# Optimization experiments

Measured on AMD Instinct MI355X. Metric: run time of the kernel, lower is better.

Reference implementation:

```python
import jax, jax.numpy as jnp
import numpy as np

B, S, D, H = 8, 2048, 256, 256


def setup_inputs() -> dict:
    key = jax.random.key(0)
    ks = jax.random.split(key, 7)
    s_ih = 1.0 / np.sqrt(D)
    s_hh = 1.0 / np.sqrt(H)
    return {
        "x": jax.random.normal(ks[0], (B, S, D), dtype=jnp.float32),
        "Wih_f": jax.random.uniform(ks[1], (4 * H, D), jnp.float32, -s_ih, s_ih),
        "bih_f": jax.random.uniform(ks[2], (4 * H,), jnp.float32, -s_ih, s_ih),
        "Whh_f": jax.random.uniform(ks[3], (4 * H, H), jnp.float32, -s_hh, s_hh),
        "Wih_b": jax.random.uniform(ks[4], (4 * H, D), jnp.float32, -s_ih, s_ih),
        "bih_b": jax.random.uniform(ks[5], (4 * H,), jnp.float32, -s_ih, s_ih),
        "Whh_b": jax.random.uniform(ks[6], (4 * H, H), jnp.float32, -s_hh, s_hh),
    }


def _lstm_dir(x, Wih, bih, Whh, reverse):
    # Precompute input projection for all timesteps in one GEMM: [B,S,4H]
    b, s, _ = x.shape
    h_dim = Whh.shape[1]
    x_proj = jnp.einsum("bsd,gd->bsg", x, Wih) + bih

    def step(carry, xt):  # xt: [B,4H]
        h, c = carry
        gates = xt + h @ Whh.T
        i, f, g, o = jnp.split(gates, 4, axis=-1)
        i = jax.nn.sigmoid(i)
        f = jax.nn.sigmoid(f)
        o = jax.nn.sigmoid(o)
        g = jnp.tanh(g)
        c = f * c + i * g
        h = o * jnp.tanh(c)
        return (h, c), h

    init = (jnp.zeros((b, h_dim), x.dtype), jnp.zeros((b, h_dim), x.dtype))
    # scan over time; reverse=True processes t=S-1..0 and stacks outputs in
    # original time order, matching the torch backward loop with insert(0, .)
    _, hs = jax.lax.scan(step, init, jnp.swapaxes(x_proj, 0, 1), reverse=reverse)
    return jnp.swapaxes(hs, 0, 1)  # [B,S,H]


def reference(x, Wih_f, bih_f, Whh_f, Wih_b, bih_b, Whh_b):
    fwd = _lstm_dir(x, Wih_f, bih_f, Whh_f, reverse=False)
    bwd = _lstm_dir(x, Wih_b, bih_b, Whh_b, reverse=True)
    return jnp.concatenate([fwd, bwd], axis=-1)  # [B,S,2H]
```

## Files before the change

kernel.cpp:

```cpp
#include <hip/hip_runtime.h>
#include <hip/hip_bf16.h>
#include <stdint.h>

#define SQ   2048
#define NB   8
#define G4   1024
#define NROW 16384

typedef float f32x4 __attribute__((ext_vector_type(4)));
typedef short bf16x8 __attribute__((ext_vector_type(8)));
typedef uint32_t u32;
typedef unsigned long long u64;

__device__ __forceinline__ f32x4 mfma16(bf16x8 a, bf16x8 b, f32x4 c) {
  return __builtin_amdgcn_mfma_f32_16x16x32_bf16(a, b, c, 0, 0, 0);
}
__device__ __forceinline__ u32 pk_bf16(float lo, float hi) {
  u32 r;
  asm("v_cvt_pk_bf16_f32 %0, %1, %2" : "=v"(r) : "v"(lo), "v"(hi));
  return r;
}
__device__ __forceinline__ float bf_lo(u32 u){ union{u32 a; float f;} x; x.a = u << 16;        return x.f; }
__device__ __forceinline__ float bf_hi(u32 u){ union{u32 a; float f;} x; x.a = u & 0xffff0000u; return x.f; }

__device__ __forceinline__ float sigm(float x)   { return 1.0f / (1.0f + __expf(-x)); }
__device__ __forceinline__ float tanh_f(float x) { return 1.0f - 2.0f / (__expf(2.0f * x) + 1.0f); }

#define PIN(x) asm volatile("" : "+v"(x))

__device__ __forceinline__ u64 ld_fast(const u64* p) {
  u64 v;
  asm volatile("global_load_dwordx2 %0, %1, off sc0\n\ts_waitcnt vmcnt(0)"
               : "=v"(v) : "v"(p) : "memory");
  return v;
}
__device__ __forceinline__ void st_fast(u64* p, u64 v) {
  asm volatile("global_store_dwordx2 %0, %1, off sc0" :: "v"(p), "v"(v) : "memory");
}

__global__ __launch_bounds__(256) void xproj_gemm(
    const float* __restrict__ x,
    const float* __restrict__ WihF, const float* __restrict__ bihF,
    const float* __restrict__ WihB, const float* __restrict__ bihB,
    uint16_t* __restrict__ xp)
{
  const int dir = blockIdx.z;
  const float* Wih = dir ? WihB : WihF;
  const float* bih = dir ? bihB : bihF;
  char* xpd = (char*)xp + (size_t)dir * ((size_t)NROW * G4 * 2);

  const int g0 = blockIdx.y * 128;
  const int m0 = blockIdx.x * 128;

  __shared__ union {
    struct { short A[128 * 72]; short B[128 * 72]; } s;
    short T[128 * 136];
  } u;
  __shared__ float biasS[128];

  const int tid  = threadIdx.x;
  const int lane = tid & 63;
  const int w    = tid >> 6;
  const int wg   = w >> 1;
  const int wm   = w & 1;
  const int l15  = lane & 15;
  const int l4   = lane >> 4;

  if (tid < 128) biasS[tid] = bih[g0 + tid];

  f32x4 acc[4][4] = {};

  const int r_st = tid >> 1;
  const int half = tid & 1;
  const int mrow_st = m0 + r_st;
  const int xb = mrow_st & 7;
  const int xt = mrow_st >> 3;
  const float* xrow = x + ((size_t)xb * SQ + xt) * 256;
  const float* wrow = Wih + (size_t)(g0 + r_st) * 256;

  for (int s = 0; s < 4; ++s) {
    const int k0 = s * 64;
    __syncthreads();
    {
      const float* srcA = wrow + k0 + half * 32;
      const float* srcB = xrow + k0 + half * 32;
      short* dstA = u.s.A + r_st * 72 + half * 32;
      short* dstB = u.s.B + r_st * 72 + half * 32;
      #pragma unroll
      for (int j = 0; j < 4; ++j) {
        f32x4 a0 = *(const f32x4*)(srcA + j * 8);
        f32x4 a1 = *(const f32x4*)(srcA + j * 8 + 4);
        uint4 pa = { pk_bf16(a0.x, a0.y), pk_bf16(a0.z, a0.w),
                     pk_bf16(a1.x, a1.y), pk_bf16(a1.z, a1.w) };
        *(uint4*)(dstA + j * 8) = pa;
        f32x4 b0 = *(const f32x4*)(srcB + j * 8);
        f32x4 b1 = *(const f32x4*)(srcB + j * 8 + 4);
        uint4 pb = { pk_bf16(b0.x, b0.y), pk_bf16(b0.z, b0.w),
                     pk_bf16(b1.x, b1.y), pk_bf16(b1.z, b1.w) };
        *(uint4*)(dstB + j * 8) = pb;
      }
    }
    __syncthreads();
    #pragma unroll
    for (int kt = 0; kt < 2; ++kt) {
      bf16x8 aF[4], bF[4];
      #pragma unroll
      for (int i = 0; i < 4; ++i) {
        const int ar = wg * 64 + i * 16 + l15;
        const int br = wm * 64 + i * 16 + l15;
        aF[i] = *(const bf16x8*)(u.s.A + ar * 72 + kt * 32 + l4 * 8);
        bF[i] = *(const bf16x8*)(u.s.B + br * 72 + kt * 32 + l4 * 8);
      }
      #pragma unroll
      for (int i = 0; i < 4; ++i)
        #pragma unroll
        for (int j = 0; j < 4; ++j)
          acc[i][j] = mfma16(aF[i], bF[j], acc[i][j]);
    }
  }

  __syncthreads();
  #pragma unroll
  for (int i = 0; i < 4; ++i) {
    const f32x4 bv = *(const f32x4*)(biasS + wg * 64 + i * 16 + l4 * 4);
    #pragma unroll
    for (int j = 0; j < 4; ++j) {
      f32x4 v = acc[i][j];
      v.x += bv.x; v.y += bv.y; v.z += bv.z; v.w += bv.w;
      const int mrow = wm * 64 + j * 16 + l15;
      const int gcol = wg * 64 + i * 16 + l4 * 4;
      uint2 p; p.x = pk_bf16(v.x, v.y); p.y = pk_bf16(v.z, v.w);
      *(uint2*)(u.T + mrow * 136 + gcol) = p;
    }
  }
  __syncthreads();
  {
    const char* trow = (const char*)(u.T + r_st * 136);
    char* orow = xpd + (size_t)(m0 + r_st) * 2048 + g0 * 2;
    #pragma unroll
    for (int j = 0; j < 8; ++j) {
      const int local = half * 128 + j * 16;
      uint4 v = *(const uint4*)(trow + local);
      *(uint4*)(orow + local) = v;
    }
  }
}

template<int HALF>
__device__ __forceinline__ void lstm_body(
    const float* __restrict__ Whh, const uint16_t* __restrict__ xpd,
    float* __restrict__ out,
    u64* exf_me, u64* exs_me, const u64* exf_pt, const u64* exs_pt, int dir,
    uint16_t (*hT)[8][136], uint16_t (*hP)[8][136])
{
  const int tid  = threadIdx.x;
  const int lane = tid & 63;
  const int w    = tid >> 6;
  const int l15  = lane & 15;
  const int l4   = lane >> 4;
  const int bcl  = lane & 7;
  const int qsel = (lane >> 3) & 1;

  bf16x8 W[4][8];
  #pragma unroll
  for (int g = 0; g < 4; ++g) {
    const int row = g * 256 + HALF * 128 + w * 16 + l15;
    const float* src = Whh + (size_t)row * 256 + l4 * 8;
    #pragma unroll
    for (int kt = 0; kt < 8; ++kt) {
      f32x4 v0 = *(const f32x4*)(src + kt * 32);
      f32x4 v1 = *(const f32x4*)(src + kt * 32 + 4);
      union { bf16x8 v; u32 u[4]; } pk;
      pk.u[0] = pk_bf16(v0.x, v0.y); pk.u[1] = pk_bf16(v0.z, v0.w);
      pk.u[2] = pk_bf16(v1.x, v1.y); pk.u[3] = pk_bf16(v1.z, v1.w);
      W[g][kt] = pk.v;
      PIN(W[g][kt]);
    }
  }

  const int d0   = w * 16 + l4 * 4 + qsel * 2;
  const int word = bcl * 64 + (d0 >> 1);
  float c0 = 0.0f, c1 = 0.0f;

  u32 xq[4], xqn[4];
  {
    const int tt0 = dir ? SQ - 1 : 0;
    const uint16_t* xr = xpd + (size_t)(tt0 * 8 + bcl) * 1024 + HALF * 128 + d0;
    #pragma unroll
    for (int g = 0; g < 4; ++g) xq[g] = *(const u32*)(xr + g * 256);
  }

  int thr = 8;
  int slowWins = 0;

  #pragma unroll 1
  for (int t = 0; t < SQ; ++t) {
    const int tt = dir ? (SQ - 1 - t) : t;

    if (t > 0) {
      const u32 want = (u32)t;
      const size_t off = (size_t)((t - 1) & 1) * 512 + tid;
      u64 pw;
      int tries = 0;
      for (;;) {
        if (tries < thr)
          pw = ld_fast(exf_pt + off);
        else
          pw = __hip_atomic_load(exs_pt + off, __ATOMIC_RELAXED,
                                 __HIP_MEMORY_SCOPE_AGENT);
        if ((u32)pw == want) break;
        ++tries;
      }
      if (thr > 0 && tries >= thr) { if (++slowWins >= 4) thr = 0; }
      *(u32*)&hP[(t - 1) & 1][w][lane * 2] = (u32)(pw >> 32);
    }
    asm volatile("s_waitcnt lgkmcnt(0)" ::: "memory");
    __builtin_amdgcn_s_barrier();

    {
      const int tn = (t + 1 < SQ) ? t + 1 : SQ - 1;
      const int ttn = dir ? (SQ - 1 - tn) : tn;
      const uint16_t* xr = xpd + (size_t)(ttn * 8 + bcl) * 1024 + HALF * 128 + d0;
      #pragma unroll
      for (int g = 0; g < 4; ++g) xqn[g] = *(const u32*)(xr + g * 256);
    }

    f32x4 acc[4] = {};
    if (t > 0) {
      #pragma unroll
      for (int ko = 0; ko < 4; ++ko) {
        const bf16x8 bO = *(const bf16x8*)&hT[t & 1][bcl][ko * 32 + l4 * 8];
        #pragma unroll
        for (int g = 0; g < 4; ++g) acc[g] = mfma16(W[g][HALF * 4 + ko], bO, acc[g]);
        const bf16x8 bP = *(const bf16x8*)&hP[(t - 1) & 1][bcl][ko * 32 + l4 * 8];
        #pragma unroll
        for (int g = 0; g < 4; ++g) acc[g] = mfma16(W[g][(1 - HALF) * 4 + ko], bP, acc[g]);
      }
    }

    float P0[4], P1[4];
    #pragma unroll
    for (int g = 0; g < 4; ++g) {
      P0[g] = (qsel ? acc[g].z : acc[g].x) + bf_lo(xq[g]);
      P1[g] = (qsel ? acc[g].w : acc[g].y) + bf_hi(xq[g]);
    }
    const float i0 = sigm(P0[0]), f0 = sigm(P0[1]), g0v = tanh_f(P0[2]), o0 = sigm(P0[3]);
    const float i1 = sigm(P1[0]), f1 = sigm(P1[1]), g1v = tanh_f(P1[2]), o1 = sigm(P1[3]);
    c0 = f0 * c0 + i0 * g0v;
    c1 = f1 * c1 + i1 * g1v;
    const float h0 = o0 * tanh_f(c0);
    const float h1 = o1 * tanh_f(c1);

    const u32 h01 = pk_bf16(h0, h1);
    const u64 pub = ((u64)h01 << 32) | (u64)(u32)(t + 1);
    st_fast(exf_me + (size_t)(t & 1) * 512 + word, pub);
    __hip_atomic_store(exs_me + (size_t)(t & 1) * 512 + word, pub,
                       __ATOMIC_RELAXED, __HIP_MEMORY_SCOPE_AGENT);
    *(u32*)&hT[(t + 1) & 1][bcl][d0] = h01;
    *(float2*)(out + ((size_t)bcl * SQ + tt) * 512 + dir * 256 + HALF * 128 + d0) =
        make_float2(h0, h1);

    #pragma unroll
    for (int g = 0; g < 4; ++g) xq[g] = xqn[g];
  }
}

__global__ __launch_bounds__(512, 2) void lstm_rec(
    const float* __restrict__ WhhF, const float* __restrict__ WhhB,
    const uint16_t* __restrict__ xp, float* __restrict__ out,
    u64* exs, u64* exf)
{
  __shared__ uint16_t hT[2][8][136];
  __shared__ uint16_t hP[2][8][136];

  const int bid  = blockIdx.x;
  const int dir  = bid & 7;
  const int half = bid >> 3;
  if (dir > 1) return;

  const float* Whh = dir ? WhhB : WhhF;
  const uint16_t* xpd = xp + (size_t)dir * NROW * G4;
  const size_t me = (size_t)(dir * 2 + half) * 1024;
  const size_t pt = (size_t)(dir * 2 + (1 - half)) * 1024;

  if (half == 0)
    lstm_body<0>(Whh, xpd, out, exf + me, exs + me, exf + pt, exs + pt, dir, hT, hP);
  else
    lstm_body<1>(Whh, xpd, out, exf + me, exs + me, exf + pt, exs + pt, dir, hT, hP);
}

extern "C" void kernel_launch(void* const* d_in, const int* in_sizes, int n_in,
                              void* d_out, int out_size, void* d_ws, size_t ws_size,
                              hipStream_t stream) {
  const float* x    = (const float*)d_in[0];
  const float* WihF = (const float*)d_in[1];
  const float* bihF = (const float*)d_in[2];
  const float* WhhF = (const float*)d_in[3];
  const float* WihB = (const float*)d_in[4];
  const float* bihB = (const float*)d_in[5];
  const float* WhhB = (const float*)d_in[6];
  float* out = (float*)d_out;

  const size_t XPB = (size_t)2 * NROW * G4 * 2;
  const size_t EXB = (size_t)4096 * sizeof(u64);
  if (ws_size < XPB + 2 * EXB) return;
  uint16_t* xpw = (uint16_t*)d_ws;
  u64* exs = (u64*)((char*)d_ws + XPB);
  u64* exf = (u64*)((char*)d_ws + XPB + EXB);

  hipMemsetAsync(exs, 0, 2 * EXB, stream);
  xproj_gemm<<<dim3(128, 8, 2), dim3(256), 0, stream>>>(x, WihF, bihF, WihB, bihB, xpw);
  lstm_rec<<<dim3(16), dim3(512), 0, stream>>>(WhhF, WhhB, xpw, out, exs, exf);
}
```

Measured before the change: 6.597 ms.

## Split each LSTM direction across four workgroups with three-peer hidden-state exchange

The recurrent kernel now splits each direction's hidden dimension over four 256-thread workgroups of 64 units each, instead of two 512-thread workgroups of 128 units. Each workgroup polls three peers' published h slices with batched sc0 loads, assembles the full 256-wide h in one LDS buffer, and runs eight K-steps of MFMA. Smaller workgroups shorten the per-step gate compute and barrier, but every step now waits on three remote peers instead of one, which adds exchange traffic and cross-CU latency to the serial critical path.

```diff
diff --git a/kernel.cpp b/kernel.cpp
--- a/kernel.cpp
+++ b/kernel.cpp
@@ -146,13 +146,21 @@
   }
 }
 
-template<int HALF>
-__device__ __forceinline__ void lstm_body(
-    const float* __restrict__ Whh, const uint16_t* __restrict__ xpd,
-    float* __restrict__ out,
-    u64* exf_me, u64* exs_me, const u64* exf_pt, const u64* exs_pt, int dir,
-    uint16_t (*hT)[8][136], uint16_t (*hP)[8][136])
+__global__ __launch_bounds__(256, 1) void lstm_rec(
+    const float* __restrict__ WhhF, const float* __restrict__ WhhB,
+    const uint16_t* __restrict__ xp, float* __restrict__ out,
+    u64* exs, u64* exf)
 {
+  __shared__ alignas(16) uint16_t hF[2][8][264];
+
+  const int bid = blockIdx.x;
+  const int dir = bid & 7;
+  const int c   = bid >> 3;
+  if (dir > 1) return;
+
+  const float* Whh = dir ? WhhB : WhhF;
+  const uint16_t* xpd = xp + (size_t)dir * NROW * G4;
+
   const int tid  = threadIdx.x;
   const int lane = tid & 63;
   const int w    = tid >> 6;
@@ -164,7 +172,7 @@
   bf16x8 W[4][8];
   #pragma unroll
   for (int g = 0; g < 4; ++g) {
-    const int row = g * 256 + HALF * 128 + w * 16 + l15;
+    const int row = g * 256 + c * 64 + w * 16 + l15;
     const float* src = Whh + (size_t)row * 256 + l4 * 8;
     #pragma unroll
     for (int kt = 0; kt < 8; ++kt) {
@@ -178,20 +186,31 @@
     }
   }
 
+  u64* exf_me = exf + (size_t)(dir * 4 + c) * 512;
+  u64* exs_me = exs + (size_t)(dir * 4 + c) * 512;
+  const u64* pf[3]; const u64* ps[3];
+  #pragma unroll
+  for (int j = 0; j < 3; ++j) {
+    const int cc = (c + 1 + j) & 3;
+    pf[j] = exf + (size_t)(dir * 4 + cc) * 512;
+    ps[j] = exs + (size_t)(dir * 4 + cc) * 512;
+  }
+  const int cc0 = ((c + 1) & 3) * 64, cc1 = ((c + 2) & 3) * 64, cc2 = ((c + 3) & 3) * 64;
+  const int sb = tid >> 5, sp2 = (tid & 31) * 2;
+
   const int d0   = w * 16 + l4 * 4 + qsel * 2;
-  const int word = bcl * 64 + (d0 >> 1);
+  const int word = bcl * 32 + (d0 >> 1);
   float c0 = 0.0f, c1 = 0.0f;
 
   u32 xq[4], xqn[4];
   {
     const int tt0 = dir ? SQ - 1 : 0;
-    const uint16_t* xr = xpd + (size_t)(tt0 * 8 + bcl) * 1024 + HALF * 128 + d0;
+    const uint16_t* xr = xpd + (size_t)(tt0 * 8 + bcl) * 1024 + c * 64 + d0;
     #pragma unroll
     for (int g = 0; g < 4; ++g) xq[g] = *(const u32*)(xr + g * 256);
   }
 
-  int thr = 8;
-  int slowWins = 0;
+  int slowMode = 0, slowWins = 0;
 
   #pragma unroll 1
   for (int t = 0; t < SQ; ++t) {
@@ -199,20 +218,44 @@
 
     if (t > 0) {
       const u32 want = (u32)t;
-      const size_t off = (size_t)((t - 1) & 1) * 512 + tid;
-      u64 pw;
-      int tries = 0;
-      for (;;) {
-        if (tries < thr)
-          pw = ld_fast(exf_pt + off);
-        else
-          pw = __hip_atomic_load(exs_pt + off, __ATOMIC_RELAXED,
-                                 __HIP_MEMORY_SCOPE_AGENT);
-        if ((u32)pw == want) break;
-        ++tries;
-      }
-      if (thr > 0 && tries >= thr) { if (++slowWins >= 4) thr = 0; }
-      *(u32*)&hP[(t - 1) & 1][w][lane * 2] = (u32)(pw >> 32);
+      const size_t soff = (size_t)((t - 1) & 1) * 256 + tid;
+      u64 pw0, pw1, pw2;
+      if (!slowMode) {
+        asm volatile(
+          "global_load_dwordx2 %0, %3, off sc0\n\t"
+          "global_load_dwordx2 %1, %4, off sc0\n\t"
+          "global_load_dwordx2 %2, %5, off sc0\n\t"
+          "s_waitcnt vmcnt(0)"
+          : "=v"(pw0), "=v"(pw1), "=v"(pw2)
+          : "v"(pf[0] + soff), "v"(pf[1] + soff), "v"(pf[2] + soff)
+          : "memory");
+      } else {
+        pw0 = __hip_atomic_load(ps[0] + soff, __ATOMIC_RELAXED, __HIP_MEMORY_SCOPE_AGENT);
+        pw1 = __hip_atomic_load(ps[1] + soff, __ATOMIC_RELAXED, __HIP_MEMORY_SCOPE_AGENT);
+        pw2 = __hip_atomic_load(ps[2] + soff, __ATOMIC_RELAXED, __HIP_MEMORY_SCOPE_AGENT);
+      }
+      int anySlow = 0;
+      #pragma unroll
+      for (int j = 0; j < 3; ++j) {
+        u64& pw = (j == 0) ? pw0 : (j == 1) ? pw1 : pw2;
+        int tries = 0;
+        while ((u32)pw != want) {
+          ++tries;
+          if (slowMode || tries > 8) {
+            anySlow = 1;
+            pw = __hip_atomic_load(ps[j] + soff, __ATOMIC_RELAXED,
+                                   __HIP_MEMORY_SCOPE_AGENT);
+          } else {
+            pw = ld_fast(pf[j] + soff);
+          }
+        }
+      }
+      if (!slowMode && anySlow) { if (++slowWins >= 4) slowMode = 1; }
+
+      uint16_t* hrow = &hF[(t - 1) & 1][sb][0];
+      *(u32*)(hrow + cc0 + sp2) = (u32)(pw0 >> 32);
+      *(u32*)(hrow + cc1 + sp2) = (u32)(pw1 >> 32);
+      *(u32*)(hrow + cc2 + sp2) = (u32)(pw2 >> 32);
     }
     asm volatile("s_waitcnt lgkmcnt(0)" ::: "memory");
     __builtin_amdgcn_s_barrier();
@@ -220,7 +263,7 @@
     {
       const int tn = (t + 1 < SQ) ? t + 1 : SQ - 1;
       const int ttn = dir ? (SQ - 1 - tn) : tn;
-      const uint16_t* xr = xpd + (size_t)(ttn * 8 + bcl) * 1024 + HALF * 128 + d0;
+      const uint16_t* xr = xpd + (size_t)(ttn * 8 + bcl) * 1024 + c * 64 + d0;
       #pragma unroll
       for (int g = 0; g < 4; ++g) xqn[g] = *(const u32*)(xr + g * 256);
     }
@@ -228,13 +271,10 @@
     f32x4 acc[4] = {};
     if (t > 0) {
       #pragma unroll
-      for (int ko = 0; ko < 4; ++ko) {
-        const bf16x8 bO = *(const bf16x8*)&hT[t & 1][bcl][ko * 32 + l4 * 8];
+      for (int kt = 0; kt < 8; ++kt) {
+        const bf16x8 bF = *(const bf16x8*)&hF[(t - 1) & 1][bcl][kt * 32 + l4 * 8];
         #pragma unroll
-        for (int g = 0; g < 4; ++g) acc[g] = mfma16(W[g][HALF * 4 + ko], bO, acc[g]);
-        const bf16x8 bP = *(const bf16x8*)&hP[(t - 1) & 1][bcl][ko * 32 + l4 * 8];
-        #pragma unroll
-        for (int g = 0; g < 4; ++g) acc[g] = mfma16(W[g][(1 - HALF) * 4 + ko], bP, acc[g]);
+        for (int g = 0; g < 4; ++g) acc[g] = mfma16(W[g][kt], bF, acc[g]);
       }
     }
 
@@ -253,40 +293,16 @@
 
     const u32 h01 = pk_bf16(h0, h1);
     const u64 pub = ((u64)h01 << 32) | (u64)(u32)(t + 1);
-    st_fast(exf_me + (size_t)(t & 1) * 512 + word, pub);
-    __hip_atomic_store(exs_me + (size_t)(t & 1) * 512 + word, pub,
+    st_fast(exf_me + (size_t)(t & 1) * 256 + word, pub);
+    __hip_atomic_store(exs_me + (size_t)(t & 1) * 256 + word, pub,
                        __ATOMIC_RELAXED, __HIP_MEMORY_SCOPE_AGENT);
-    *(u32*)&hT[(t + 1) & 1][bcl][d0] = h01;
-    *(float2*)(out + ((size_t)bcl * SQ + tt) * 512 + dir * 256 + HALF * 128 + d0) =
+    *(u32*)&hF[t & 1][bcl][c * 64 + d0] = h01;
+    *(float2*)(out + ((size_t)bcl * SQ + tt) * 512 + dir * 256 + c * 64 + d0) =
         make_float2(h0, h1);
 
     #pragma unroll
     for (int g = 0; g < 4; ++g) xq[g] = xqn[g];
   }
-}
-
-__global__ __launch_bounds__(512, 2) void lstm_rec(
-    const float* __restrict__ WhhF, const float* __restrict__ WhhB,
-    const uint16_t* __restrict__ xp, float* __restrict__ out,
-    u64* exs, u64* exf)
-{
-  __shared__ uint16_t hT[2][8][136];
-  __shared__ uint16_t hP[2][8][136];
-
-  const int bid  = blockIdx.x;
-  const int dir  = bid & 7;
-  const int half = bid >> 3;
-  if (dir > 1) return;
-
-  const float* Whh = dir ? WhhB : WhhF;
-  const uint16_t* xpd = xp + (size_t)dir * NROW * G4;
-  const size_t me = (size_t)(dir * 2 + half) * 1024;
-  const size_t pt = (size_t)(dir * 2 + (1 - half)) * 1024;
-
-  if (half == 0)
-    lstm_body<0>(Whh, xpd, out, exf + me, exs + me, exf + pt, exs + pt, dir, hT, hP);
-  else
-    lstm_body<1>(Whh, xpd, out, exf + me, exs + me, exf + pt, exs + pt, dir, hT, hP);
 }
 
 extern "C" void kernel_launch(void* const* d_in, const int* in_sizes, int n_in,
@@ -310,5 +326,5 @@
 
   hipMemsetAsync(exs, 0, 2 * EXB, stream);
   xproj_gemm<<<dim3(128, 8, 2), dim3(256), 0, stream>>>(x, WihF, bihF, WihB, bihB, xpw);
-  lstm_rec<<<dim3(16), dim3(512), 0, stream>>>(WhhF, WhhB, xpw, out, exs, exf);
-}
+  lstm_rec<<<dim3(32), dim3(256), 0, stream>>>(WhhF, WhhB, xpw, out, exs, exf);
+}
```

Result: faster. 6.079 ms (-7.9%).
